# Kernel tuning notes

Hardware: AMD Instinct MI355X
Metric: run time of the kernel (lower is better)

Reference implementation:

```python
import jax, jax.numpy as jnp
import numpy as np
import math

B, S, H = 4, 2048, 1024
EMBED_DIM = 1024


def setup_inputs() -> dict:
    key = jax.random.key(0)
    ks = jax.random.split(key, 7)
    scale = 1.0 / math.sqrt(H)
    return {
        "xs": jax.random.normal(ks[0], (B, S, H), dtype=jnp.float32),
        "WQ_w": jax.random.normal(ks[1], (EMBED_DIM, H), dtype=jnp.float32) * scale,
        "WQ_b": jax.random.normal(ks[2], (EMBED_DIM,), dtype=jnp.float32) * scale,
        "WK_w": jax.random.normal(ks[3], (EMBED_DIM, H), dtype=jnp.float32) * scale,
        "WK_b": jax.random.normal(ks[4], (EMBED_DIM,), dtype=jnp.float32) * scale,
        "WV_w": jax.random.normal(ks[5], (EMBED_DIM, H), dtype=jnp.float32) * scale,
        "WV_b": jax.random.normal(ks[6], (EMBED_DIM,), dtype=jnp.float32) * scale,
    }


def reference(xs, WQ_w, WQ_b, WK_w, WK_b, WV_w, WV_b):
    # Linear projections (torch nn.Linear: x @ W.T + b)
    q = jnp.einsum('bsh,eh->bse', xs, WQ_w) + WQ_b  # [B,S,E]
    k = jnp.einsum('bsh,eh->bse', xs, WK_w) + WK_b
    v = jnp.einsum('bsh,eh->bse', xs, WV_w) + WV_b
    seq_len = xs.shape[1]
    inv_sqrt_e = 1.0 / math.sqrt(EMBED_DIM)
    qk = jnp.einsum('bqe,bke->bqk', q, k) * inv_sqrt_e  # [B,S,S]
    # causal mask: positions k > q get -inf (triu, diagonal=1)
    causal = jnp.tril(jnp.ones((seq_len, seq_len), dtype=bool))
    qk = jnp.where(causal[None, :, :], qk, -jnp.inf)
    attn = jax.nn.softmax(qk, axis=2)
    y = jnp.einsum('bqk,bke->bqe', attn, v)  # [B,S,E]
    return y
```

## Files before the change

kernel.cpp:

```cpp
#include <hip/hip_runtime.h>
#include <cstdint>
#include <cstddef>

typedef _Float16 f16;
typedef __attribute__((ext_vector_type(4))) _Float16 f16x4;
typedef __attribute__((ext_vector_type(8))) _Float16 f16x8;
typedef __attribute__((ext_vector_type(4))) float f32x4;

static constexpr int BB = 4;
static constexpr int SS = 2048;
static constexpr int EE = 1024;

static constexpr int BM = 128, BN = 128, BK = 32;

__device__ __forceinline__ void gload_lds16(const f16* g, f16* l) {
  __builtin_amdgcn_global_load_lds(
      (const __attribute__((address_space(1))) void*)g,
      (__attribute__((address_space(3))) void*)l, 16, 0, 0);
}

struct Frag {
  int lane, wave, wy, wx, l16, quad;
  __device__ Frag() {
    const int tid = threadIdx.x;
    lane = tid & 63; wave = tid >> 6;
    wy = wave >> 1; wx = wave & 1;
    l16 = lane & 15; quad = lane >> 4;
  }
};

__device__ __forceinline__ void gemm_core(
    const f16* __restrict__ A, const f16* __restrict__ Bt,
    int lda, int ldb, int kTiles,
    f16* __restrict__ Ash, f16* __restrict__ Bsh,
    f32x4 acc[4][4], const Frag& fr)
{
  const int ca0 = fr.wave * 128 + fr.lane;
  const int ca1 = ca0 + 64;
  const int ra0 = ca0 >> 2, ka0 = (ca0 & 3) << 3;
  const int ra1 = ca1 >> 2, ka1 = (ca1 & 3) << 3;

  const f16* gA0 = A + (size_t)ra0 * lda + ka0;
  const f16* gA1 = A + (size_t)ra1 * lda + ka1;
  const f16* gB0 = Bt + (size_t)ra0 * ldb + ka0;
  const f16* gB1 = Bt + (size_t)ra1 * ldb + ka1;
  f16* lA0 = Ash + ca0 * 8;
  f16* lA1 = Ash + ca1 * 8;
  f16* lB0 = Bsh + ca0 * 8;
  f16* lB1 = Bsh + ca1 * 8;

  for (int kt = 0; kt < kTiles; ++kt) {
    const int ko = kt * BK;
    gload_lds16(gA0 + ko, lA0);
    gload_lds16(gA1 + ko, lA1);
    gload_lds16(gB0 + ko, lB0);
    gload_lds16(gB1 + ko, lB1);
    __syncthreads();
    f16x8 af[4], bf[4];
#pragma unroll
    for (int mi = 0; mi < 4; ++mi)
      af[mi] = *(const f16x8*)(Ash + (fr.wy * 64 + mi * 16 + fr.l16) * BK + fr.quad * 8);
#pragma unroll
    for (int ni = 0; ni < 4; ++ni)
      bf[ni] = *(const f16x8*)(Bsh + (fr.wx * 64 + ni * 16 + fr.l16) * BK + fr.quad * 8);
#pragma unroll
    for (int mi = 0; mi < 4; ++mi)
#pragma unroll
      for (int ni = 0; ni < 4; ++ni)
        acc[mi][ni] = __builtin_amdgcn_mfma_f32_16x16x32_f16(af[mi], bf[ni], acc[mi][ni], 0, 0, 0);
    __syncthreads();
  }
}

__global__ __launch_bounds__(256) void cast_kernel(
    const float* __restrict__ in, f16* __restrict__ out, int n4)
{
  const int i = blockIdx.x * 256 + threadIdx.x;
  if (i < n4) {
    const float4 f = ((const float4*)in)[i];
    f16x4 h;
    h.x = (f16)f.x; h.y = (f16)f.y; h.z = (f16)f.z; h.w = (f16)f.w;
    ((f16x4*)out)[i] = h;
  }
}

__global__ __launch_bounds__(256, 2) void qkv_kernel(
    const f16* __restrict__ X,
    const f16* __restrict__ W0, const f16* __restrict__ W1, const f16* __restrict__ W2,
    const float* __restrict__ b0, const float* __restrict__ b1, const float* __restrict__ b2,
    f16* __restrict__ O0, f16* __restrict__ O1, f16* __restrict__ O2)
{
  __shared__ __align__(16) f16 Ash[BM * BK];
  __shared__ __align__(16) f16 Bsh[BN * BK];
  const int z = blockIdx.z;
  const f16* W = (z == 0) ? W0 : (z == 1) ? W1 : W2;
  const float* bias = (z == 0) ? b0 : (z == 1) ? b1 : b2;
  f16* out = (z == 0) ? O0 : (z == 1) ? O1 : O2;
  const int row0 = blockIdx.x * BM, col0 = blockIdx.y * BN;
  Frag fr;
  f32x4 acc[4][4] = {};
  gemm_core(X + (size_t)row0 * EE, W + (size_t)col0 * EE, EE, EE, EE / BK, Ash, Bsh, acc, fr);
#pragma unroll
  for (int ni = 0; ni < 4; ++ni) {
    const int c = col0 + fr.wx * 64 + ni * 16 + fr.l16;
    const float bv = bias[c];
#pragma unroll
    for (int mi = 0; mi < 4; ++mi) {
      const int r = row0 + fr.wy * 64 + mi * 16 + fr.quad * 4;
#pragma unroll
      for (int i = 0; i < 4; ++i)
        out[(size_t)(r + i) * EE + c] = (f16)(acc[mi][ni][i] + bv);
    }
  }
}

__global__ __launch_bounds__(256) void transpose_kernel(
    const f16* __restrict__ V, f16* __restrict__ Vt)
{
  __shared__ __align__(16) f16 t[64][68];
  const int b = blockIdx.z;
  const int s0 = blockIdx.x * 64, e0 = blockIdx.y * 64;
  const int tid = threadIdx.x;
  const int r = tid >> 4;
  const int c4 = (tid & 15) << 2;
  const f16* src = V + (size_t)b * SS * EE;
  f16* dst = Vt + (size_t)b * EE * SS;
#pragma unroll
  for (int i = 0; i < 4; ++i) {
    const int row = i * 16 + r;
    const f16x4 v = *(const f16x4*)(src + (size_t)(s0 + row) * EE + e0 + c4);
    *(f16x4*)&t[row][c4] = v;
  }
  __syncthreads();
#pragma unroll
  for (int i = 0; i < 4; ++i) {
    const int row = i * 16 + r;
    f16x4 v;
    v.x = t[c4 + 0][row]; v.y = t[c4 + 1][row];
    v.z = t[c4 + 2][row]; v.w = t[c4 + 3][row];
    *(f16x4*)(dst + (size_t)(e0 + row) * SS + s0 + c4) = v;
  }
}

__global__ __launch_bounds__(256, 2) void scores_kernel(
    const f16* __restrict__ Q, const f16* __restrict__ Kh, f16* __restrict__ Sc)
{
  __shared__ __align__(16) f16 Ash[BM * BK];
  __shared__ __align__(16) f16 Bsh[BN * BK];
  const int qt = blockIdx.x, kt = blockIdx.y, b = blockIdx.z;
  if (kt > qt) return;
  const f16* A  = Q  + (size_t)b * SS * EE + (size_t)qt * BM * EE;
  const f16* Bp = Kh + (size_t)b * SS * EE + (size_t)kt * BN * EE;
  f16* out = Sc + (size_t)b * SS * SS;
  Frag fr;
  f32x4 acc[4][4] = {};
  gemm_core(A, Bp, EE, EE, EE / BK, Ash, Bsh, acc, fr);
  const float scale = 0.03125f;
#pragma unroll
  for (int ni = 0; ni < 4; ++ni) {
    const int c = kt * BN + fr.wx * 64 + ni * 16 + fr.l16;
#pragma unroll
    for (int mi = 0; mi < 4; ++mi) {
      const int r = qt * BM + fr.wy * 64 + mi * 16 + fr.quad * 4;
#pragma unroll
      for (int i = 0; i < 4; ++i)
        out[(size_t)(r + i) * SS + c] = (f16)(acc[mi][ni][i] * scale);
    }
  }
}

__global__ __launch_bounds__(256) void softmax_kernel(f16* __restrict__ Sc)
{
  const int q = blockIdx.x, b = blockIdx.y;
  f16* row = Sc + (size_t)b * SS * SS + (size_t)q * SS;
  const int n = q + 1;
  const int tid = threadIdx.x;
  float v[8];
  float m = -1e30f;
  int cnt = 0;
  for (int i = tid; i < n; i += 256) { const float s = (float)row[i]; v[cnt++] = s; m = fmaxf(m, s); }
  __shared__ float red[4];
#pragma unroll
  for (int off = 32; off > 0; off >>= 1) m = fmaxf(m, __shfl_down(m, off));
  if ((tid & 63) == 0) red[tid >> 6] = m;
  __syncthreads();
  m = fmaxf(fmaxf(red[0], red[1]), fmaxf(red[2], red[3]));
  float sum = 0.f;
  for (int j = 0; j < cnt; ++j) { v[j] = __expf(v[j] - m); sum += v[j]; }
#pragma unroll
  for (int off = 32; off > 0; off >>= 1) sum += __shfl_down(sum, off);
  __syncthreads();
  if ((tid & 63) == 0) red[tid >> 6] = sum;
  __syncthreads();
  sum = red[0] + red[1] + red[2] + red[3];
  const float inv = 1.f / sum;
  cnt = 0;
  for (int i = tid; i < n; i += 256) row[i] = (f16)(v[cnt++] * inv);
  const int kend = ((q >> 7) + 1) << 7;
  for (int i = n + tid; i < kend; i += 256) row[i] = (f16)0.f;
}

__global__ __launch_bounds__(256, 2) void pv_kernel(
    const f16* __restrict__ P, const f16* __restrict__ Vt, float* __restrict__ Y)
{
  __shared__ __align__(16) f16 Ash[BM * BK];
  __shared__ __align__(16) f16 Bsh[BN * BK];
  const int qt = blockIdx.x, et = blockIdx.y, b = blockIdx.z;
  const f16* A  = P  + (size_t)b * SS * SS + (size_t)qt * BM * SS;
  const f16* Bp = Vt + (size_t)b * EE * SS + (size_t)et * BN * SS;
  float* out = Y + (size_t)b * SS * EE;
  Frag fr;
  f32x4 acc[4][4] = {};
  gemm_core(A, Bp, SS, SS, (qt + 1) * (BM / BK), Ash, Bsh, acc, fr);
#pragma unroll
  for (int ni = 0; ni < 4; ++ni) {
    const int c = et * BN + fr.wx * 64 + ni * 16 + fr.l16;
#pragma unroll
    for (int mi = 0; mi < 4; ++mi) {
      const int r = qt * BM + fr.wy * 64 + mi * 16 + fr.quad * 4;
#pragma unroll
      for (int i = 0; i < 4; ++i)
        out[(size_t)(r + i) * EE + c] = acc[mi][ni][i];
    }
  }
}

extern "C" void kernel_launch(void* const* d_in, const int* in_sizes, int n_in,
                              void* d_out, int out_size, void* d_ws, size_t ws_size,
                              hipStream_t stream)
{
  const float* xs  = (const float*)d_in[0];
  const float* WQw = (const float*)d_in[1];
  const float* WQb = (const float*)d_in[2];
  const float* WKw = (const float*)d_in[3];
  const float* WKb = (const float*)d_in[4];
  const float* WVw = (const float*)d_in[5];
  const float* WVb = (const float*)d_in[6];

  const size_t ME = (size_t)BB * SS * EE;
  const size_t WE = (size_t)EE * EE;

  f16* Xh = (f16*)d_ws;
  f16* Wq = Xh + ME;
  f16* Wk = Wq + WE;
  f16* Wv = Wk + WE;
  f16* Qh = Wv + WE;
  f16* Kh = Qh + ME;
  f16* Vh = Kh + ME;
  f16* Vt = Vh + ME;
  f16* Sc = Vt + ME;

  cast_kernel<<<dim3((unsigned)(ME / 4 / 256)), 256, 0, stream>>>(xs, Xh, (int)(ME / 4));
  cast_kernel<<<dim3((unsigned)(WE / 4 / 256)), 256, 0, stream>>>(WQw, Wq, (int)(WE / 4));
  cast_kernel<<<dim3((unsigned)(WE / 4 / 256)), 256, 0, stream>>>(WKw, Wk, (int)(WE / 4));
  cast_kernel<<<dim3((unsigned)(WE / 4 / 256)), 256, 0, stream>>>(WVw, Wv, (int)(WE / 4));

  qkv_kernel<<<dim3((BB * SS) / BM, EE / BN, 3), 256, 0, stream>>>(
      Xh, Wq, Wk, Wv, WQb, WKb, WVb, Qh, Kh, Vh);
  transpose_kernel<<<dim3(SS / 64, EE / 64, BB), 256, 0, stream>>>(Vh, Vt);
  scores_kernel<<<dim3(SS / BM, SS / BN, BB), 256, 0, stream>>>(Qh, Kh, Sc);
  softmax_kernel<<<dim3(SS, BB), 256, 0, stream>>>(Sc);
  pv_kernel<<<dim3(SS / BM, EE / BN, BB), 256, 0, stream>>>(Sc, Vt, (float*)d_out);
}
```

Measured before the change: 287.5 us.

## Merge weight casts, compact causal grid, vectorize softmax, reorder PV tiles, raise occupancy

Combines the three weight-cast launches into one kernel. Launches the scores GEMM over only the lower-triangular tiles instead of exiting early in the upper ones. Rewrites softmax to load and store 8 halves per thread as vectors. Reverses the PV tile order so the longest causal tiles start first, and raises the launch_bounds occupancy hint from 2 to 4 on the GEMM kernels. The higher occupancy target may force register spilling in the 4x4 MFMA accumulator kernels.

```diff
diff --git a/kernel.cpp b/kernel.cpp
--- a/kernel.cpp
+++ b/kernel.cpp
@@ -84,7 +84,23 @@
   }
 }
 
-__global__ __launch_bounds__(256, 2) void qkv_kernel(
+__global__ __launch_bounds__(256) void cast_w_kernel(
+    const float* __restrict__ w0, const float* __restrict__ w1, const float* __restrict__ w2,
+    f16* __restrict__ o0, f16* __restrict__ o1, f16* __restrict__ o2, int n4)
+{
+  const int z = blockIdx.y;
+  const float* in = (z == 0) ? w0 : (z == 1) ? w1 : w2;
+  f16* out = (z == 0) ? o0 : (z == 1) ? o1 : o2;
+  const int i = blockIdx.x * 256 + threadIdx.x;
+  if (i < n4) {
+    const float4 f = ((const float4*)in)[i];
+    f16x4 h;
+    h.x = (f16)f.x; h.y = (f16)f.y; h.z = (f16)f.z; h.w = (f16)f.w;
+    ((f16x4*)out)[i] = h;
+  }
+}
+
+__global__ __launch_bounds__(256, 4) void qkv_kernel(
     const f16* __restrict__ X,
     const f16* __restrict__ W0, const f16* __restrict__ W1, const f16* __restrict__ W2,
     const float* __restrict__ b0, const float* __restrict__ b1, const float* __restrict__ b2,
@@ -142,13 +158,15 @@
   }
 }
 
-__global__ __launch_bounds__(256, 2) void scores_kernel(
+__global__ __launch_bounds__(256, 4) void scores_kernel(
     const f16* __restrict__ Q, const f16* __restrict__ Kh, f16* __restrict__ Sc)
 {
   __shared__ __align__(16) f16 Ash[BM * BK];
   __shared__ __align__(16) f16 Bsh[BN * BK];
-  const int qt = blockIdx.x, kt = blockIdx.y, b = blockIdx.z;
-  if (kt > qt) return;
+  const int t = blockIdx.x, b = blockIdx.z;
+  int qt = 0;
+  while ((qt + 1) * (qt + 2) / 2 <= t) ++qt;
+  const int kt = t - qt * (qt + 1) / 2;
   const f16* A  = Q  + (size_t)b * SS * EE + (size_t)qt * BM * EE;
   const f16* Bp = Kh + (size_t)b * SS * EE + (size_t)kt * BN * EE;
   f16* out = Sc + (size_t)b * SS * SS;
@@ -174,19 +192,39 @@
   const int q = blockIdx.x, b = blockIdx.y;
   f16* row = Sc + (size_t)b * SS * SS + (size_t)q * SS;
   const int n = q + 1;
+  const int kend = ((q >> 7) + 1) << 7;
   const int tid = threadIdx.x;
+  const int i0 = tid * 8;
+
   float v[8];
-  float m = -1e30f;
-  int cnt = 0;
-  for (int i = tid; i < n; i += 256) { const float s = (float)row[i]; v[cnt++] = s; m = fmaxf(m, s); }
+  if (i0 + 8 <= n) {
+    const f16x8 h = *(const f16x8*)(row + i0);
+#pragma unroll
+    for (int j = 0; j < 8; ++j) v[j] = (float)h[j];
+  } else {
+#pragma unroll
+    for (int j = 0; j < 8; ++j) {
+      const int idx = i0 + j;
+      v[j] = (idx < n) ? (float)row[idx] : -1e30f;
+    }
+  }
+
+  float m = v[0];
+#pragma unroll
+  for (int j = 1; j < 8; ++j) m = fmaxf(m, v[j]);
   __shared__ float red[4];
 #pragma unroll
   for (int off = 32; off > 0; off >>= 1) m = fmaxf(m, __shfl_down(m, off));
   if ((tid & 63) == 0) red[tid >> 6] = m;
   __syncthreads();
   m = fmaxf(fmaxf(red[0], red[1]), fmaxf(red[2], red[3]));
+
   float sum = 0.f;
-  for (int j = 0; j < cnt; ++j) { v[j] = __expf(v[j] - m); sum += v[j]; }
+#pragma unroll
+  for (int j = 0; j < 8; ++j) {
+    v[j] = (i0 + j < n) ? __expf(v[j] - m) : 0.f;
+    sum += v[j];
+  }
 #pragma unroll
   for (int off = 32; off > 0; off >>= 1) sum += __shfl_down(sum, off);
   __syncthreads();
@@ -194,18 +232,21 @@
   __syncthreads();
   sum = red[0] + red[1] + red[2] + red[3];
   const float inv = 1.f / sum;
-  cnt = 0;
-  for (int i = tid; i < n; i += 256) row[i] = (f16)(v[cnt++] * inv);
-  const int kend = ((q >> 7) + 1) << 7;
-  for (int i = n + tid; i < kend; i += 256) row[i] = (f16)0.f;
-}
-
-__global__ __launch_bounds__(256, 2) void pv_kernel(
+
+  if (i0 < kend) {
+    f16x8 h;
+#pragma unroll
+    for (int j = 0; j < 8; ++j) h[j] = (f16)(v[j] * inv);
+    *(f16x8*)(row + i0) = h;
+  }
+}
+
+__global__ __launch_bounds__(256, 4) void pv_kernel(
     const f16* __restrict__ P, const f16* __restrict__ Vt, float* __restrict__ Y)
 {
   __shared__ __align__(16) f16 Ash[BM * BK];
   __shared__ __align__(16) f16 Bsh[BN * BK];
-  const int qt = blockIdx.x, et = blockIdx.y, b = blockIdx.z;
+  const int qt = (gridDim.x - 1) - blockIdx.x, et = blockIdx.y, b = blockIdx.z;
   const f16* A  = P  + (size_t)b * SS * SS + (size_t)qt * BM * SS;
   const f16* Bp = Vt + (size_t)b * EE * SS + (size_t)et * BN * SS;
   float* out = Y + (size_t)b * SS * EE;
@@ -251,14 +292,14 @@
   f16* Sc = Vt + ME;
 
   cast_kernel<<<dim3((unsigned)(ME / 4 / 256)), 256, 0, stream>>>(xs, Xh, (int)(ME / 4));
-  cast_kernel<<<dim3((unsigned)(WE / 4 / 256)), 256, 0, stream>>>(WQw, Wq, (int)(WE / 4));
-  cast_kernel<<<dim3((unsigned)(WE / 4 / 256)), 256, 0, stream>>>(WKw, Wk, (int)(WE / 4));
-  cast_kernel<<<dim3((unsigned)(WE / 4 / 256)), 256, 0, stream>>>(WVw, Wv, (int)(WE / 4));
+  cast_w_kernel<<<dim3((unsigned)(WE / 4 / 256), 3), 256, 0, stream>>>(
+      WQw, WKw, WVw, Wq, Wk, Wv, (int)(WE / 4));
 
   qkv_kernel<<<dim3((BB * SS) / BM, EE / BN, 3), 256, 0, stream>>>(
       Xh, Wq, Wk, Wv, WQb, WKb, WVb, Qh, Kh, Vh);
   transpose_kernel<<<dim3(SS / 64, EE / 64, BB), 256, 0, stream>>>(Vh, Vt);
-  scores_kernel<<<dim3(SS / BM, SS / BN, BB), 256, 0, stream>>>(Qh, Kh, Sc);
+  const int nTri = (SS / BM) * (SS / BM + 1) / 2;
+  scores_kernel<<<dim3(nTri, 1, BB), 256, 0, stream>>>(Qh, Kh, Sc);
   softmax_kernel<<<dim3(SS, BB), 256, 0, stream>>>(Sc);
   pv_kernel<<<dim3(SS / BM, EE / BN, BB), 256, 0, stream>>>(Sc, Vt, (float*)d_out);
 }
```

Measured after the change: 267.8 us. -6.9%, faster.
